# Kernel optimization log

Hardware: AMD Instinct MI355X
Metric: run time of the kernel (lower is better)

## Reference

```python
import jax, jax.numpy as jnp
import numpy as np

EMBED_DIM = 1024
NUM_HEADS = 16
D_K = EMBED_DIM // NUM_HEADS


def setup_inputs() -> dict:
    key = jax.random.key(0)
    kx, kq, kk, kv, ko = jax.random.split(key, 5)
    scale = 1.0 / np.sqrt(EMBED_DIM)
    x = jax.random.normal(kx, (4, 2048, EMBED_DIM), dtype=jnp.float32)
    # Linear(embed_dim, embed_dim, bias=False) weights, stored [out, in] like torch
    Wq = jax.random.uniform(kq, (EMBED_DIM, EMBED_DIM), jnp.float32, -scale, scale)
    Wk = jax.random.uniform(kk, (EMBED_DIM, EMBED_DIM), jnp.float32, -scale, scale)
    Wv = jax.random.uniform(kv, (EMBED_DIM, EMBED_DIM), jnp.float32, -scale, scale)
    Wo = jax.random.uniform(ko, (EMBED_DIM, EMBED_DIM), jnp.float32, -scale, scale)
    return {"x": x, "Wq": Wq, "Wk": Wk, "Wv": Wv, "Wo": Wo}


def reference(x, Wq, Wk, Wv, Wo):
    b, s, _ = x.shape
    # torch Linear: y = x @ W.T
    def proj(W):
        y = jnp.einsum('bse,fe->bsf', x, W)
        return y.reshape(b, s, NUM_HEADS, D_K).transpose(0, 2, 1, 3)  # [b,h,s,d]
    q, k, v = proj(Wq), proj(Wk), proj(Wv)
    scores = jnp.einsum('bhqd,bhkd->bhqk', q, k) / jnp.sqrt(jnp.float32(D_K))
    attn = jax.nn.softmax(scores, axis=-1)  # dropout is identity in eval
    out = jnp.einsum('bhqk,bhkd->bhqd', attn, v)
    out = out.transpose(0, 2, 1, 3).reshape(b, s, EMBED_DIM)
    return jnp.einsum('bsf,ef->bse', out, Wo)
```

## Files before the change

kernel.cpp:

```cpp
#include <hip/hip_runtime.h>
#include <hip/hip_bf16.h>

typedef unsigned short u16;
typedef unsigned int   u32;
typedef __attribute__((ext_vector_type(8))) __bf16 bf16x8;
typedef __attribute__((ext_vector_type(2))) __bf16 bf16x2;
typedef __attribute__((ext_vector_type(8))) u16    ushort8v;
typedef __attribute__((ext_vector_type(2))) float  f32x2;
typedef __attribute__((ext_vector_type(4))) float  floatx4;

#define EMBED 1024
#define SEQ   2048
#define BATCH 4
#define NH    16
#define DKH   64
#define BHN   (BATCH*NH)
#define ZSTRIDE ((size_t)BHN*SEQ*DKH)

__device__ __forceinline__ u16 f2bf(float f){
  union { float f; unsigned u; } v; v.f = f;
  unsigned r = (v.u + 0x7FFFu + ((v.u >> 16) & 1u)) >> 16;
  return (u16)r;
}
__device__ __forceinline__ u32 pk2(float a, float b){
  f32x2 v = {a, b};
  return __builtin_bit_cast(u32, __builtin_convertvector(v, bf16x2));
}

__device__ __forceinline__ bf16x8 ld_frag(const u16* p){
  return __builtin_bit_cast(bf16x8, *(const ushort8v*)p);
}

__device__ __forceinline__ floatx4 mfma16(bf16x8 a, bf16x8 b, floatx4 c){
  return __builtin_amdgcn_mfma_f32_16x16x32_bf16(a, b, c, 0, 0, 0);
}

__device__ __forceinline__ void gl_lds16(const u16* g, u16* l){
  __builtin_amdgcn_global_load_lds((const __attribute__((address_space(1))) void*)g,
                                   (__attribute__((address_space(3))) void*)l,
                                   16, 0, 0);
}

__global__ __launch_bounds__(256) void cvt_all(const float* __restrict__ x,
    const float* __restrict__ wq, const float* __restrict__ wk,
    const float* __restrict__ wv, const float* __restrict__ wo,
    u16* __restrict__ Xb, u16* __restrict__ Wqb, u16* __restrict__ Wkb,
    u16* __restrict__ Wvb, u16* __restrict__ Wob){
  int b = blockIdx.x;
  const float* src; u16* dst; int i;
  if (b < 8192){ src = x; dst = Xb; i = b*256 + threadIdx.x; }
  else {
    int k = (b - 8192) >> 10, r = (b - 8192) & 1023;
    src = (k==0) ? wq : (k==1) ? wk : (k==2) ? wv : wo;
    dst = (k==0) ? Wqb : (k==1) ? Wkb : (k==2) ? Wvb : Wob;
    i = r*256 + threadIdx.x;
  }
  float4 v = ((const float4*)src)[i];
  ushort4 o;
  o.x = f2bf(v.x); o.y = f2bf(v.y); o.z = f2bf(v.z); o.w = f2bf(v.w);
  ((ushort4*)dst)[i] = o;
}

__device__ __forceinline__ void gemm_core_db(const u16* Abase, const u16* Bbase,
                                             u16* As, u16* Bs, floatx4 acc[4][4]){
  const int tid  = threadIdx.x;
  const int lane = tid & 63, w = tid >> 6;
  const int lm   = lane & 15, quad = lane >> 4;
  const int wm   = (w & 1) * 64, wn = (w >> 1) * 64;
  const int row0 = tid >> 2, kc = tid & 3;
  const int row1 = (256 + tid) >> 2;

  #pragma unroll
  for (int mi = 0; mi < 4; ++mi)
    #pragma unroll
    for (int ni = 0; ni < 4; ++ni)
      acc[mi][ni] = (floatx4){0.f, 0.f, 0.f, 0.f};

  gl_lds16(Abase + (size_t)row0*EMBED + kc*8, As + tid*8);
  gl_lds16(Bbase + (size_t)row0*EMBED + kc*8, Bs + tid*8);
  gl_lds16(Abase + (size_t)row1*EMBED + kc*8, As + (256 + tid)*8);
  gl_lds16(Bbase + (size_t)row1*EMBED + kc*8, Bs + (256 + tid)*8);

  for (int kt = 0; kt < EMBED/32; ++kt){
    const int cur = kt & 1;
    __syncthreads();
    if (kt + 1 < EMBED/32){
      const int k0 = (kt + 1) * 32;
      u16* Ad = As + (cur^1)*128*32;
      u16* Bd = Bs + (cur^1)*128*32;
      gl_lds16(Abase + (size_t)row0*EMBED + k0 + kc*8, Ad + tid*8);
      gl_lds16(Bbase + (size_t)row0*EMBED + k0 + kc*8, Bd + tid*8);
      gl_lds16(Abase + (size_t)row1*EMBED + k0 + kc*8, Ad + (256 + tid)*8);
      gl_lds16(Bbase + (size_t)row1*EMBED + k0 + kc*8, Bd + (256 + tid)*8);
    }
    const u16* Ac = As + cur*128*32;
    const u16* Bc = Bs + cur*128*32;
    bf16x8 af[4], bf[4];
    #pragma unroll
    for (int mi = 0; mi < 4; ++mi)
      af[mi] = ld_frag(&Ac[(wm + mi*16 + lm)*32 + quad*8]);
    #pragma unroll
    for (int ni = 0; ni < 4; ++ni)
      bf[ni] = ld_frag(&Bc[(wn + ni*16 + lm)*32 + quad*8]);
    #pragma unroll
    for (int mi = 0; mi < 4; ++mi)
      #pragma unroll
      for (int ni = 0; ni < 4; ++ni)
        acc[mi][ni] = mfma16(af[mi], bf[ni], acc[mi][ni]);
  }
}

#define QSCALE 0.1803368801111204f
__global__ __launch_bounds__(256, 2) void gemm_qkv(const u16* __restrict__ X,
    const u16* __restrict__ Wq, const u16* __restrict__ Wk, const u16* __restrict__ Wv,
    u16* __restrict__ QKV){
  __shared__ __attribute__((aligned(16))) u16 As[2*128*32];
  __shared__ __attribute__((aligned(16))) u16 Bs[3][2*128*32];

  const int tid = threadIdx.x, lane = tid & 63, w = tid >> 6;
  const int lm = lane & 15, quad = lane >> 4;
  const int wm = (w & 1) * 64, wn = (w >> 1) * 64;
  const int m0 = blockIdx.x * 128, n0 = blockIdx.y * 128;
  const int row0 = tid >> 2, kc = tid & 3;

  const u16* A0 = X  + (size_t)(m0 + row0)*EMBED + kc*8;
  const u16* B0[3] = {
    Wq + (size_t)(n0 + row0)*EMBED + kc*8,
    Wk + (size_t)(n0 + row0)*EMBED + kc*8,
    Wv + (size_t)(n0 + row0)*EMBED + kc*8 };

  floatx4 acc[3][4][4];
  #pragma unroll
  for (int z = 0; z < 3; ++z)
    #pragma unroll
    for (int mi = 0; mi < 4; ++mi)
      #pragma unroll
      for (int ni = 0; ni < 4; ++ni)
        acc[z][mi][ni] = (floatx4){0.f, 0.f, 0.f, 0.f};

  gl_lds16(A0,             As + tid*8);
  gl_lds16(A0 + 64*EMBED,  As + (256 + tid)*8);
  #pragma unroll
  for (int z = 0; z < 3; ++z){
    gl_lds16(B0[z],            Bs[z] + tid*8);
    gl_lds16(B0[z] + 64*EMBED, Bs[z] + (256 + tid)*8);
  }

  for (int kt = 0; kt < EMBED/32; ++kt){
    const int cur = kt & 1;
    __syncthreads();
    if (kt + 1 < EMBED/32){
      const int k0 = (kt + 1) * 32;
      gl_lds16(A0 + k0,            As + (cur^1)*4096 + tid*8);
      gl_lds16(A0 + 64*EMBED + k0, As + (cur^1)*4096 + (256 + tid)*8);
      #pragma unroll
      for (int z = 0; z < 3; ++z){
        gl_lds16(B0[z] + k0,            Bs[z] + (cur^1)*4096 + tid*8);
        gl_lds16(B0[z] + 64*EMBED + k0, Bs[z] + (cur^1)*4096 + (256 + tid)*8);
      }
    }
    const u16* Ac = As + cur*4096;
    bf16x8 af[4];
    #pragma unroll
    for (int mi = 0; mi < 4; ++mi)
      af[mi] = ld_frag(&Ac[(wm + mi*16 + lm)*32 + quad*8]);
    #pragma unroll
    for (int z = 0; z < 3; ++z){
      const u16* Bc = Bs[z] + cur*4096;
      bf16x8 bfz[4];
      #pragma unroll
      for (int ni = 0; ni < 4; ++ni)
        bfz[ni] = ld_frag(&Bc[(wn + ni*16 + lm)*32 + quad*8]);
      #pragma unroll
      for (int mi = 0; mi < 4; ++mi)
        #pragma unroll
        for (int ni = 0; ni < 4; ++ni)
          acc[z][mi][ni] = mfma16(af[mi], bfz[ni], acc[z][mi][ni]);
    }
  }

  #pragma unroll
  for (int z = 0; z < 2; ++z){
    const float scale = (z == 0) ? QSCALE : 1.0f;
    u16* outz = QKV + (size_t)z * ZSTRIDE;
    #pragma unroll
    for (int mi = 0; mi < 4; ++mi)
      #pragma unroll
      for (int ni = 0; ni < 4; ++ni)
        #pragma unroll
        for (int r = 0; r < 4; ++r){
          int m = m0 + wm + mi*16 + quad*4 + r;
          int n = n0 + wn + ni*16 + lm;
          int b = m >> 11, s = m & 2047, h = n >> 6, d = n & 63;
          outz[(((size_t)(b*NH + h))*SEQ + s)*DKH + d] = f2bf(acc[z][mi][ni][r] * scale);
        }
  }
  {
    u16* outz = QKV + (size_t)2 * ZSTRIDE;
    #pragma unroll
    for (int mi = 0; mi < 4; ++mi)
      #pragma unroll
      for (int ni = 0; ni < 4; ++ni){
        int mbase = m0 + wm + mi*16 + quad*4;
        int n = n0 + wn + ni*16 + lm;
        int b = mbase >> 11, sb = mbase & 2047;
        int h = n >> 6, d = n & 63;
        u16* dst = outz + (((size_t)(b*NH + h))*DKH + d)*SEQ + sb;
        uint2 pv;
        pv.x = pk2(acc[2][mi][ni][0], acc[2][mi][ni][1]);
        pv.y = pk2(acc[2][mi][ni][2], acc[2][mi][ni][3]);
        *reinterpret_cast<uint2*>(dst) = pv;
      }
  }
}

__global__ __launch_bounds__(256) void gemm_out(const u16* __restrict__ A,
    const u16* __restrict__ W, float* __restrict__ C){
  __shared__ __attribute__((aligned(16))) u16 As[2*128*32];
  __shared__ __attribute__((aligned(16))) u16 Bs[2*128*32];
  const int m0 = blockIdx.x * 128, n0 = blockIdx.y * 128;
  floatx4 acc[4][4];
  gemm_core_db(A + (size_t)m0*EMBED, W + (size_t)n0*EMBED, As, Bs, acc);

  const int tid = threadIdx.x, lane = tid & 63, w = tid >> 6;
  const int lm = lane & 15, quad = lane >> 4;
  const int wm = (w & 1) * 64, wn = (w >> 1) * 64;
  #pragma unroll
  for (int mi = 0; mi < 4; ++mi)
    #pragma unroll
    for (int ni = 0; ni < 4; ++ni)
      #pragma unroll
      for (int r = 0; r < 4; ++r){
        int m = m0 + wm + mi*16 + quad*4 + r;
        int n = n0 + wn + ni*16 + lm;
        C[(size_t)m*EMBED + n] = acc[mi][ni][r];
      }
}

#define KSS 520
__global__ __launch_bounds__(256, 4) void attn_kernel(const u16* __restrict__ QKV,
                                                      u16* __restrict__ Out){
  __shared__ __attribute__((aligned(16))) u16 Ks[2][8*KSS];
  __shared__ __attribute__((aligned(16))) u16 Vs[2][64*64];

  const int tid = threadIdx.x, lane = tid & 63, w = tid >> 6;
  const int lm = lane & 15, quad = lane >> 4;
  const int bh = blockIdx.x;
  const int q0 = blockIdx.y * 128;
  const u16* Qh = QKV + (size_t)bh * SEQ * DKH;
  const u16* Kh = QKV + ZSTRIDE + (size_t)bh * SEQ * DKH;
  const u16* Vh = QKV + 2*ZSTRIDE + (size_t)bh * DKH * SEQ;

  const int sK = tid & 63, cK = tid >> 6;
  const int dV = tid >> 3, gV = tid & 7;
  const size_t vsrc0 = (size_t)dV * SEQ + ((gV ^ (dV & 7)) * 8);
  const size_t vsrc1 = vsrc0 + (size_t)32 * SEQ;

  bf16x8 qf[2][2];
  #pragma unroll
  for (int qt = 0; qt < 2; ++qt)
    #pragma unroll
    for (int st = 0; st < 2; ++st)
      qf[qt][st] = ld_frag(Qh + (size_t)(q0 + w*32 + qt*16 + lm)*DKH + st*32 + quad*8);

  const uint4 ONESW = {0x3F803F80u, 0x3F803F80u, 0x3F803F80u, 0x3F803F80u};
  const bf16x8 ones8 = __builtin_bit_cast(bf16x8, ONESW);

  floatx4 o[2][4], lac[2];
  #pragma unroll
  for (int qt = 0; qt < 2; ++qt){
    lac[qt] = (floatx4){0.f, 0.f, 0.f, 0.f};
    #pragma unroll
    for (int dt = 0; dt < 4; ++dt) o[qt][dt] = (floatx4){0.f, 0.f, 0.f, 0.f};
  }

  gl_lds16(Kh + (size_t)sK*DKH + cK*8,     Ks[0] + cK*KSS + sK*8);
  gl_lds16(Kh + (size_t)sK*DKH + (cK+4)*8, Ks[0] + (cK+4)*KSS + sK*8);
  gl_lds16(Vh + vsrc0,                     Vs[0] + tid*8);
  gl_lds16(Vh + vsrc1,                     Vs[0] + 2048 + tid*8);

  for (int kt = 0; kt < SEQ/64; ++kt){
    const int cur = kt & 1;
    __syncthreads();
    if (kt + 1 < SEQ/64){
      const int nk0 = (kt + 1) * 64;
      gl_lds16(Kh + (size_t)(nk0 + sK)*DKH + cK*8,     Ks[cur^1] + cK*KSS + sK*8);
      gl_lds16(Kh + (size_t)(nk0 + sK)*DKH + (cK+4)*8, Ks[cur^1] + (cK+4)*KSS + sK*8);
      gl_lds16(Vh + vsrc0 + nk0,                       Vs[cur^1] + tid*8);
      gl_lds16(Vh + vsrc1 + nk0,                       Vs[cur^1] + 2048 + tid*8);
    }
    const u16* Kc = Ks[cur];
    const u16* Vc = Vs[cur];

    #pragma unroll
    for (int u = 0; u < 2; ++u){
      uint2 ph[2][2];
      #pragma unroll
      for (int half = 0; half < 2; ++half){
        const int t = u*2 + half;
        bf16x8 kf0 = ld_frag(&Kc[quad*KSS     + (t*16 + lm)*8]);
        bf16x8 kf1 = ld_frag(&Kc[(quad+4)*KSS + (t*16 + lm)*8]);
        #pragma unroll
        for (int qt = 0; qt < 2; ++qt){
          floatx4 s = (floatx4){0.f,0.f,0.f,0.f};
          __builtin_amdgcn_s_setprio(1);
          s = mfma16(kf0, qf[qt][0], s);
          s = mfma16(kf1, qf[qt][1], s);
          __builtin_amdgcn_s_setprio(0);
          ph[qt][half].x = pk2(__builtin_amdgcn_exp2f(s[0]), __builtin_amdgcn_exp2f(s[1]));
          ph[qt][half].y = pk2(__builtin_amdgcn_exp2f(s[2]), __builtin_amdgcn_exp2f(s[3]));
        }
      }
      bf16x8 pf[2];
      #pragma unroll
      for (int qt = 0; qt < 2; ++qt){
        uint4 pp = {ph[qt][0].x, ph[qt][0].y, ph[qt][1].x, ph[qt][1].y};
        pf[qt] = __builtin_bit_cast(bf16x8, pp);
      }
      const int cg0 = (((u*4     + (quad >> 1)) ^ (lm & 7)) * 8) + (quad & 1) * 4;
      const int cg1 = (((u*4 + 2 + (quad >> 1)) ^ (lm & 7)) * 8) + (quad & 1) * 4;
      __builtin_amdgcn_s_setprio(1);
      lac[0] = mfma16(pf[0], ones8, lac[0]);
      lac[1] = mfma16(pf[1], ones8, lac[1]);
      #pragma unroll
      for (int dt = 0; dt < 4; ++dt){
        uint2 vlo = *(const uint2*)(Vc + (dt*16 + lm)*64 + cg0);
        uint2 vhi = *(const uint2*)(Vc + (dt*16 + lm)*64 + cg1);
        uint4 vv = {vlo.x, vlo.y, vhi.x, vhi.y};
        bf16x8 vb = __builtin_bit_cast(bf16x8, vv);
        o[0][dt] = mfma16(pf[0], vb, o[0][dt]);
        o[1][dt] = mfma16(pf[1], vb, o[1][dt]);
      }
      __builtin_amdgcn_s_setprio(0);
    }
  }

  const int bI = bh >> 4, h = bh & 15;
  #pragma unroll
  for (int qt = 0; qt < 2; ++qt){
    floatx4 inv;
    #pragma unroll
    for (int r = 0; r < 4; ++r) inv[r] = __builtin_amdgcn_rcpf(lac[qt][r]);
    #pragma unroll
    for (int dt = 0; dt < 4; ++dt)
      #pragma unroll
      for (int r = 0; r < 4; ++r){
        int s = q0 + w*32 + qt*16 + quad*4 + r;
        Out[((size_t)(bI*SEQ + s))*EMBED + h*DKH + dt*16 + lm] = f2bf(o[qt][dt][r] * inv[r]);
      }
  }
}

extern "C" void kernel_launch(void* const* d_in, const int* in_sizes, int n_in,
                              void* d_out, int out_size, void* d_ws, size_t ws_size,
                              hipStream_t stream){
  const float* x  = (const float*)d_in[0];
  const float* Wq = (const float*)d_in[1];
  const float* Wk = (const float*)d_in[2];
  const float* Wv = (const float*)d_in[3];
  const float* Wo = (const float*)d_in[4];
  float* out = (float*)d_out;

  char* ws = (char*)d_ws;
  u16* Xb  = (u16*)ws;
  u16* Wqb = (u16*)(ws + (size_t)16777216);
  u16* Wkb = Wqb + 1048576;
  u16* Wvb = Wkb + 1048576;
  u16* Wob = Wvb + 1048576;
  u16* QKV = (u16*)(ws + (size_t)25165824);
  u16* At  = (u16*)(ws + (size_t)75497472);

  cvt_all<<<12288, 256, 0, stream>>>(x, Wq, Wk, Wv, Wo, Xb, Wqb, Wkb, Wvb, Wob);
  gemm_qkv<<<dim3(64, 8), 256, 0, stream>>>(Xb, Wqb, Wkb, Wvb, QKV);
  attn_kernel<<<dim3(64, 16), 256, 0, stream>>>(QKV, At);
  gemm_out<<<dim3(64, 8), 256, 0, stream>>>(At, Wob, out);
}
```

Baseline: 253.1 us.

## Fuse fp32-to-bf16 conversion of x into QKV GEMM A-tile loads

```diff
diff --git a/kernel.cpp b/kernel.cpp
--- a/kernel.cpp
+++ b/kernel.cpp
@@ -40,21 +40,22 @@
                                    (__attribute__((address_space(3))) void*)l,
                                    16, 0, 0);
 }
-
-__global__ __launch_bounds__(256) void cvt_all(const float* __restrict__ x,
+__device__ __forceinline__ void gl_lds16f(const float* g, float* l){
+  __builtin_amdgcn_global_load_lds((const __attribute__((address_space(1))) void*)g,
+                                   (__attribute__((address_space(3))) void*)l,
+                                   16, 0, 0);
+}
+
+__global__ __launch_bounds__(256) void cvt_w(
     const float* __restrict__ wq, const float* __restrict__ wk,
     const float* __restrict__ wv, const float* __restrict__ wo,
-    u16* __restrict__ Xb, u16* __restrict__ Wqb, u16* __restrict__ Wkb,
+    u16* __restrict__ Wqb, u16* __restrict__ Wkb,
     u16* __restrict__ Wvb, u16* __restrict__ Wob){
   int b = blockIdx.x;
-  const float* src; u16* dst; int i;
-  if (b < 8192){ src = x; dst = Xb; i = b*256 + threadIdx.x; }
-  else {
-    int k = (b - 8192) >> 10, r = (b - 8192) & 1023;
-    src = (k==0) ? wq : (k==1) ? wk : (k==2) ? wv : wo;
-    dst = (k==0) ? Wqb : (k==1) ? Wkb : (k==2) ? Wvb : Wob;
-    i = r*256 + threadIdx.x;
-  }
+  int k = b >> 10, r = b & 1023;
+  const float* src = (k==0) ? wq : (k==1) ? wk : (k==2) ? wv : wo;
+  u16* dst = (k==0) ? Wqb : (k==1) ? Wkb : (k==2) ? Wvb : Wob;
+  int i = r*256 + threadIdx.x;
   float4 v = ((const float4*)src)[i];
   ushort4 o;
   o.x = f2bf(v.x); o.y = f2bf(v.y); o.z = f2bf(v.z); o.w = f2bf(v.w);
@@ -111,23 +112,26 @@
 }
 
 #define QSCALE 0.1803368801111204f
-__global__ __launch_bounds__(256, 2) void gemm_qkv(const u16* __restrict__ X,
+__global__ __launch_bounds__(256, 2) void gemm_qkv(const float* __restrict__ X,
     const u16* __restrict__ Wq, const u16* __restrict__ Wk, const u16* __restrict__ Wv,
     u16* __restrict__ QKV){
-  __shared__ __attribute__((aligned(16))) u16 As[2*128*32];
-  __shared__ __attribute__((aligned(16))) u16 Bs[3][2*128*32];
+  __shared__ __attribute__((aligned(16))) float Asf[2*128*32];
+  __shared__ __attribute__((aligned(16))) u16   Bs[3][2*128*32];
 
   const int tid = threadIdx.x, lane = tid & 63, w = tid >> 6;
   const int lm = lane & 15, quad = lane >> 4;
   const int wm = (w & 1) * 64, wn = (w >> 1) * 64;
   const int m0 = blockIdx.x * 128, n0 = blockIdx.y * 128;
-  const int row0 = tid >> 2, kc = tid & 3;
-
-  const u16* A0 = X  + (size_t)(m0 + row0)*EMBED + kc*8;
+  const int rowB = tid >> 2, kcB = tid & 3;
+
+  const int arow = tid >> 3;
+  const int aoff = ((tid & 7) ^ (arow & 7)) * 4;
+  const float* A0 = X + (size_t)(m0 + arow)*EMBED + aoff;
+
   const u16* B0[3] = {
-    Wq + (size_t)(n0 + row0)*EMBED + kc*8,
-    Wk + (size_t)(n0 + row0)*EMBED + kc*8,
-    Wv + (size_t)(n0 + row0)*EMBED + kc*8 };
+    Wq + (size_t)(n0 + rowB)*EMBED + kcB*8,
+    Wk + (size_t)(n0 + rowB)*EMBED + kcB*8,
+    Wv + (size_t)(n0 + rowB)*EMBED + kcB*8 };
 
   floatx4 acc[3][4][4];
   #pragma unroll
@@ -138,8 +142,9 @@
       for (int ni = 0; ni < 4; ++ni)
         acc[z][mi][ni] = (floatx4){0.f, 0.f, 0.f, 0.f};
 
-  gl_lds16(A0,             As + tid*8);
-  gl_lds16(A0 + 64*EMBED,  As + (256 + tid)*8);
+  #pragma unroll
+  for (int r = 0; r < 4; ++r)
+    gl_lds16f(A0 + (size_t)r*32*EMBED, Asf + (r*256 + tid)*4);
   #pragma unroll
   for (int z = 0; z < 3; ++z){
     gl_lds16(B0[z],            Bs[z] + tid*8);
@@ -151,19 +156,28 @@
     __syncthreads();
     if (kt + 1 < EMBED/32){
       const int k0 = (kt + 1) * 32;
-      gl_lds16(A0 + k0,            As + (cur^1)*4096 + tid*8);
-      gl_lds16(A0 + 64*EMBED + k0, As + (cur^1)*4096 + (256 + tid)*8);
+      #pragma unroll
+      for (int r = 0; r < 4; ++r)
+        gl_lds16f(A0 + (size_t)r*32*EMBED + k0, Asf + (cur^1)*4096 + (r*256 + tid)*4);
       #pragma unroll
       for (int z = 0; z < 3; ++z){
         gl_lds16(B0[z] + k0,            Bs[z] + (cur^1)*4096 + tid*8);
         gl_lds16(B0[z] + 64*EMBED + k0, Bs[z] + (cur^1)*4096 + (256 + tid)*8);
       }
     }
-    const u16* Ac = As + cur*4096;
+    const float* Acf = Asf + cur*4096;
     bf16x8 af[4];
     #pragma unroll
-    for (int mi = 0; mi < 4; ++mi)
-      af[mi] = ld_frag(&Ac[(wm + mi*16 + lm)*32 + quad*8]);
+    for (int mi = 0; mi < 4; ++mi){
+      const int R = wm + mi*16 + lm;
+      const int u0 = (quad*2)     ^ (lm & 7);
+      const int u1 = (quad*2 + 1) ^ (lm & 7);
+      floatx4 a0 = *(const floatx4*)(Acf + R*32 + u0*4);
+      floatx4 a1 = *(const floatx4*)(Acf + R*32 + u1*4);
+      uint4 ap = { pk2(a0[0],a0[1]), pk2(a0[2],a0[3]),
+                   pk2(a1[0],a1[1]), pk2(a1[2],a1[3]) };
+      af[mi] = __builtin_bit_cast(bf16x8, ap);
+    }
     #pragma unroll
     for (int z = 0; z < 3; ++z){
       const u16* Bc = Bs[z] + cur*4096;
@@ -362,7 +376,6 @@
   float* out = (float*)d_out;
 
   char* ws = (char*)d_ws;
-  u16* Xb  = (u16*)ws;
   u16* Wqb = (u16*)(ws + (size_t)16777216);
   u16* Wkb = Wqb + 1048576;
   u16* Wvb = Wkb + 1048576;
@@ -370,8 +383,8 @@
   u16* QKV = (u16*)(ws + (size_t)25165824);
   u16* At  = (u16*)(ws + (size_t)75497472);
 
-  cvt_all<<<12288, 256, 0, stream>>>(x, Wq, Wk, Wv, Wo, Xb, Wqb, Wkb, Wvb, Wob);
-  gemm_qkv<<<dim3(64, 8), 256, 0, stream>>>(Xb, Wqb, Wkb, Wvb, QKV);
+  cvt_w<<<4096, 256, 0, stream>>>(Wq, Wk, Wv, Wo, Wqb, Wkb, Wvb, Wob);
+  gemm_qkv<<<dim3(64, 8), 256, 0, stream>>>(x, Wqb, Wkb, Wvb, QKV);
   attn_kernel<<<dim3(64, 16), 256, 0, stream>>>(QKV, At);
   gemm_out<<<dim3(64, 8), 256, 0, stream>>>(At, Wob, out);
 }
```

Result: no change. 256.8 us (+1.4%).
